# Kernel tuning notes

Hardware: AMD Instinct MI355X
Metric: run time of the kernel (lower is better)

## Reference

```python
import jax, jax.numpy as jnp
import numpy as np
import heapq

N = 256          # num nodes (also num start-node runs)
T = 5 * N        # message budget per run (graph.num_nodes * 5)
IN = 128         # in_features
H = 256          # hidden
M = 128          # message_size
OUT = 64         # out_features
E = 768          # directed edge list length (undirected adjacency built from it)


def _build_schedule(edge_index, n, t_max, rng):
    """Deterministically replay the heap simulation from the torch module.
    Returns proc[n,T] (node popped at each step), parent[n,T] (index of the
    step whose output message is consumed; -1 => first_message), valid[n,T]."""
    adj = [set() for _ in range(n)]
    src, dst = edge_index
    for s, d in zip(src, dst):
        adj[int(s)].add(int(d))
        adj[int(d)].add(int(s))
    adj = [sorted(a) for a in adj]
    proc = np.zeros((n, t_max), np.int32)
    parent = np.full((n, t_max), -1, np.int32)
    valid = np.zeros((n, t_max), bool)
    for i in range(n):
        heap = [(0.0, 0, i, -1)]  # (delay, tiebreak, node, parent_step)
        cnt = 1
        t = 0
        while heap and t < t_max:
            delay, _, node, par = heapq.heappop(heap)
            proc[i, t] = node
            parent[i, t] = par
            valid[i, t] = True
            for nb in adj[node]:
                nd = max(1e-10, rng.normal(0.5, 0.5))
                heapq.heappush(heap, (delay + nd, cnt, nb, t))
                cnt += 1
            t += 1
    return proc, parent, valid


def setup_inputs() -> dict:
    key = jax.random.key(0)
    ks = jax.random.split(key, 12)
    rng = np.random.default_rng(0)
    edge_index = rng.integers(0, N, size=(2, E))
    proc, parent, valid = _build_schedule(edge_index, N, T, rng)
    s = 0.05
    return {
        "x": jax.random.normal(ks[0], (N, IN), jnp.float32),
        "first_message": jnp.zeros((1, M), jnp.float32),
        "We": jax.random.normal(ks[1], (H, IN), jnp.float32) * s,
        "be": jax.random.normal(ks[2], (H,), jnp.float32) * s,
        "Ws": jax.random.normal(ks[3], (H, H + M), jnp.float32) * s,
        "bs": jax.random.normal(ks[4], (H,), jnp.float32) * s,
        "Wm": jax.random.normal(ks[5], (M, H + M), jnp.float32) * s,
        "bm": jax.random.normal(ks[6], (M,), jnp.float32) * s,
        "Wd": jax.random.normal(ks[7], (OUT, H), jnp.float32) * s,
        "bd": jax.random.normal(ks[8], (OUT,), jnp.float32) * s,
        "proc": jnp.asarray(proc),
        "parent": jnp.asarray(parent),
        "valid": jnp.asarray(valid),
    }


def reference(x, first_message, We, be, Ws, bs, Wm, bm, Wd, bd, proc, parent, valid):
    n = x.shape[0]
    t_max = proc.shape[1]
    m = first_message.shape[1]
    pred0 = x @ We.T + be  # encoder, recomputed fresh for every run -> shared [N,H]
    fmsg = first_message[0]

    def run(proc_i, parent_i, valid_i):
        msgs0 = jnp.zeros((t_max, m), x.dtype)

        def step(carry, inp):
            pred, msgs = carry
            t, node, par, v = inp
            msg = jnp.where(par < 0, fmsg, msgs[jnp.maximum(par, 0)])
            ns = jax.nn.relu(Ws @ jnp.concatenate([pred[node], msg]) + bs)
            nm = Wm @ jnp.concatenate([ns, msg]) + bm
            pred = pred.at[node].set(jnp.where(v, ns, pred[node]))
            msgs = msgs.at[t].set(jnp.where(v, nm, msgs[t]))
            return (pred, msgs), None

        (pred, _), _ = jax.lax.scan(
            step, (pred0, msgs0), (jnp.arange(t_max), proc_i, parent_i, valid_i)
        )
        return pred

    preds = jax.vmap(run)(proc, parent, valid)  # [N, N, H]
    diag = preds[jnp.arange(n), jnp.arange(n)]  # node i's state after run started at i
    return jax.nn.log_softmax(diag @ Wd.T + bd, axis=-1)  # [N, OUT]
```

## Files before the change

### kernel.cpp

```cpp
#include <hip/hip_runtime.h>
#include <stdint.h>

typedef _Float16 half_t;
typedef _Float16 half2_t __attribute__((ext_vector_type(2)));
typedef _Float16 half8_t __attribute__((ext_vector_type(8)));

#define NN   256
#define TT   1280
#define INF  128
#define HH   256
#define MM   128
#define OUTF 64
#define HM   384

#define THREADS 512

#define LDS_PRED    0
#define LDS_PROC    131072
#define LDS_PARENT  136192
#define LDS_FMSG    141312
#define LDS_V2      141568
#define LDS_DIAG32  143104
#define SMEM_BYTES  144128

#define WS_PRED0    0
#define WS_WSH      131072
#define WS_WMH      327680
#define WS_MSGS     425984

__device__ __forceinline__ float dot2f(half2_t a, half2_t b, float c) {
#if __has_builtin(__builtin_amdgcn_fdot2)
  return __builtin_amdgcn_fdot2(a, b, c, false);
#else
  return c + (float)a[0] * (float)b[0] + (float)a[1] * (float)b[1];
#endif
}

__global__ __launch_bounds__(256)
void prep_kernel(const float* __restrict__ Ws, const float* __restrict__ Wm,
                 half_t* __restrict__ WsH, half_t* __restrict__ WmH)
{
  const int i = blockIdx.x * 256 + threadIdx.x;
  if (i < HH * HM) WsH[i] = (half_t)Ws[i];
  else             WmH[i - HH * HM] = (half_t)Wm[i - HH * HM];
}

__global__ __launch_bounds__(256)
void enc_kernel(const float* __restrict__ x, const float* __restrict__ We,
                const float* __restrict__ be, half_t* __restrict__ pred0)
{
  __shared__ float xs[INF];
  const int n = blockIdx.x;
  const int hh = threadIdx.x;
  if (hh < INF) xs[hh] = x[n * INF + hh];
  __syncthreads();
  const float* w = We + hh * INF;
  float acc = be[hh];
#pragma unroll 16
  for (int k = 0; k < INF; ++k) acc += w[k] * xs[k];
  pred0[n * HH + hh] = (half_t)acc;
}

#define P1_CHUNK(BASE, WOFF)                                                   \
  _Pragma("unroll")                                                            \
  for (int j = 0; j < 8; ++j) {                                                \
    half8_t v = *(const half8_t*)((BASE) + j * 16);                            \
    a0 = dot2f(__builtin_shufflevector(v, v, 0, 1), w1[(WOFF) + j*4 + 0], a0); \
    a1 = dot2f(__builtin_shufflevector(v, v, 2, 3), w1[(WOFF) + j*4 + 1], a1); \
    a2 = dot2f(__builtin_shufflevector(v, v, 4, 5), w1[(WOFF) + j*4 + 2], a2); \
    a3 = dot2f(__builtin_shufflevector(v, v, 6, 7), w1[(WOFF) + j*4 + 3], a3); \
  }

__global__ __launch_bounds__(THREADS, 2)
void sim_kernel(const half_t* __restrict__ WsH, const float* __restrict__ bs,
                const half_t* __restrict__ WmH, const float* __restrict__ bm,
                const float* __restrict__ Wd, const float* __restrict__ bd,
                const float* __restrict__ fmsg,
                const int* __restrict__ proc, const int* __restrict__ parent,
                const half_t* __restrict__ pred0,
                half_t* __restrict__ msgs,
                float* __restrict__ out)
{
  extern __shared__ char smem[];
  half_t* lds_pred        = (half_t*)(smem + LDS_PRED);
  int* lds_proc           = (int*)(smem + LDS_PROC);
  int* lds_par            = (int*)(smem + LDS_PARENT);
  half_t* lds_fmsg        = (half_t*)(smem + LDS_FMSG);
  char* v2base            = smem + LDS_V2;
  float* lds_diag         = (float*)(smem + LDS_DIAG32);

  const int tid = threadIdx.x;
  const int run = blockIdx.x;
  const int r1 = tid >> 1, h = tid & 1;
  const int r2 = tid >> 2, q = tid & 3;

  half2_t w1[96];
  {
    const half8_t* wr = (const half8_t*)(WsH + r1 * HM + h * 192);
#pragma unroll
    for (int j = 0; j < 24; ++j) {
      half8_t v = wr[j];
      w1[4*j+0] = __builtin_shufflevector(v, v, 0, 1);
      w1[4*j+1] = __builtin_shufflevector(v, v, 2, 3);
      w1[4*j+2] = __builtin_shufflevector(v, v, 4, 5);
      w1[4*j+3] = __builtin_shufflevector(v, v, 6, 7);
    }
  }
  half2_t w2[48];
  {
    const half8_t* wr = (const half8_t*)(WmH + r2 * HM + q * 96);
#pragma unroll
    for (int j = 0; j < 12; ++j) {
      half8_t v = wr[j];
      w2[4*j+0] = __builtin_shufflevector(v, v, 0, 1);
      w2[4*j+1] = __builtin_shufflevector(v, v, 2, 3);
      w2[4*j+2] = __builtin_shufflevector(v, v, 4, 5);
      w2[4*j+3] = __builtin_shufflevector(v, v, 6, 7);
    }
  }
  const float bsv = bs[r1];
  const float bmv = bm[r2];

  {
    const uint4* s = (const uint4*)pred0;
    uint4* d = (uint4*)lds_pred;
#pragma unroll
    for (int i = 0; i < (NN * HH * 2 / 16) / THREADS; ++i)
      d[tid + i * THREADS] = s[tid + i * THREADS];
  }
  {
    const int* procR = proc + run * TT;
    const int* parR  = parent + run * TT;
    for (int i = tid; i < TT; i += THREADS) {
      lds_proc[i] = procR[i];
      lds_par[i]  = parR[i];
    }
  }
  if (tid < MM) lds_fmsg[tid] = (half_t)fmsg[tid];
  __syncthreads();

  float diag_reg = (h == 0) ? (float)lds_pred[run * HH + r1] : 0.f;
  half_t* msgs_run = msgs + (size_t)run * TT * MM;

  {
    const int p0 = lds_par[0];
    if (tid < 16) {
      uint4 v;
      if (p0 < 0) v = *(const uint4*)((const char*)lds_fmsg + tid * 16);
      else        v = *(const uint4*)((const char*)(msgs_run + (size_t)p0 * MM) + tid * 16);
      *(uint4*)(v2base + 512 + tid * 16) = v;
    }
  }
  __syncthreads();

  uint4 pfB = make_uint4(0, 0, 0, 0);

  int b = 0;
  for (int t = 0; t < TT; ++t, b ^= 1) {
    const int node  = lds_proc[t];
    const int vld   = (t == 0) | (lds_par[t] >= 0);
    const int parn1 = (t + 1 < TT) ? lds_par[t + 1] : -1;
    const int parn2 = (t + 2 < TT) ? lds_par[t + 2] : -1;

    const bool useA = (parn1 >= 0) && (parn1 == t - 1);
    uint4 pfA;
    if (tid < 16 && useA)
      pfA = *(const uint4*)((const char*)(msgs_run + (size_t)parn1 * MM) + tid * 16);

    const char* predrow = (const char*)(lds_pred + node * HH);
    const char* msgb    = v2base + b * 768 + 512;
    const char* b0 = h ? predrow + 384 : predrow;
    const char* b1 = h ? msgb          : predrow + 128;
    const char* b2 = h ? msgb + 128    : predrow + 256;

    float a0 = 0.f, a1 = 0.f, a2 = 0.f, a3 = 0.f;
    P1_CHUNK(b0, 0)
    P1_CHUNK(b1, 32)
    P1_CHUNK(b2, 64)
    float acc = (a0 + a1) + (a2 + a3);
    acc += __shfl_xor(acc, 1);
    const float ns_v = fmaxf(acc + bsv, 0.f);
    if (h == 0) {
      *((half_t*)(v2base + b * 768) + r1) = (half_t)ns_v;
      if (vld && node == run) diag_reg = ns_v;
    }

    if (t + 1 < TT && tid < 16) {
      char* dst = v2base + (b ^ 1) * 768 + 512 + tid * 16;
      if (parn1 < 0)
        *(uint4*)dst = *(const uint4*)((const char*)lds_fmsg + tid * 16);
      else if (parn1 != t)
        *(uint4*)dst = useA ? pfA : pfB;
    }

    if (tid < 16 && parn2 >= 0 && parn2 < t)
      pfB = *(const uint4*)((const char*)(msgs_run + (size_t)parn2 * MM) + tid * 16);

    __syncthreads();

    const char* vb = v2base + b * 768 + q * 192;
    float c0 = 0.f, c1 = 0.f, c2 = 0.f, c3 = 0.f;
#pragma unroll
    for (int j = 0; j < 12; ++j) {
      half8_t v = *(const half8_t*)(vb + j * 16);
      c0 = dot2f(__builtin_shufflevector(v, v, 0, 1), w2[j*4 + 0], c0);
      c1 = dot2f(__builtin_shufflevector(v, v, 2, 3), w2[j*4 + 1], c1);
      c2 = dot2f(__builtin_shufflevector(v, v, 4, 5), w2[j*4 + 2], c2);
      c3 = dot2f(__builtin_shufflevector(v, v, 6, 7), w2[j*4 + 3], c3);
    }
    float acc2 = (c0 + c1) + (c2 + c3);
    acc2 += __shfl_xor(acc2, 1);
    acc2 += __shfl_xor(acc2, 2);

    if (q == 0) {
      const float nm = acc2 + bmv;
      const half_t nmh = vld ? (half_t)nm : (half_t)0.f;
      if (vld) msgs_run[(size_t)t * MM + r2] = nmh;
      if (parn1 == t)
        *((half_t*)(v2base + (b ^ 1) * 768 + 512) + r2) = nmh;
    }
    if (h == 0 && vld)
      lds_pred[node * HH + r1] = (half_t)ns_v;
    __syncthreads();
  }

  if (h == 0) lds_diag[r1] = diag_reg;
  __syncthreads();

  if (tid < OUTF) {
    const float* wd = Wd + tid * HH;
    float acc = bd[tid];
#pragma unroll 8
    for (int k = 0; k < HH; ++k) acc += wd[k] * lds_diag[k];
    float m = acc;
#pragma unroll
    for (int off = 32; off >= 1; off >>= 1) m = fmaxf(m, __shfl_xor(m, off));
    const float e = __expf(acc - m);
    float s = e;
#pragma unroll
    for (int off = 32; off >= 1; off >>= 1) s += __shfl_xor(s, off);
    out[run * OUTF + tid] = acc - m - logf(s);
  }
}

extern "C" void kernel_launch(void* const* d_in, const int* in_sizes, int n_in,
                              void* d_out, int out_size, void* d_ws, size_t ws_size,
                              hipStream_t stream) {
  (void)in_sizes; (void)n_in; (void)out_size; (void)ws_size;
  const float* x    = (const float*)d_in[0];
  const float* fm   = (const float*)d_in[1];
  const float* We   = (const float*)d_in[2];
  const float* be   = (const float*)d_in[3];
  const float* Ws   = (const float*)d_in[4];
  const float* bs   = (const float*)d_in[5];
  const float* Wm   = (const float*)d_in[6];
  const float* bm   = (const float*)d_in[7];
  const float* Wd   = (const float*)d_in[8];
  const float* bd   = (const float*)d_in[9];
  const int* proc   = (const int*)d_in[10];
  const int* parent = (const int*)d_in[11];
  float* out = (float*)d_out;

  half_t* pred0 = (half_t*)((char*)d_ws + WS_PRED0);
  half_t* WsH   = (half_t*)((char*)d_ws + WS_WSH);
  half_t* WmH   = (half_t*)((char*)d_ws + WS_WMH);
  half_t* msgs  = (half_t*)((char*)d_ws + WS_MSGS);

  (void)hipFuncSetAttribute((const void*)sim_kernel,
                            hipFuncAttributeMaxDynamicSharedMemorySize, SMEM_BYTES);

  prep_kernel<<<dim3((HH * HM + MM * HM) / 256), dim3(256), 0, stream>>>(Ws, Wm, WsH, WmH);
  enc_kernel<<<dim3(NN), dim3(256), 0, stream>>>(x, We, be, pred0);
  sim_kernel<<<dim3(NN), dim3(THREADS), SMEM_BYTES, stream>>>(
      WsH, bs, WmH, bm, Wd, bd, fm, proc, parent, pred0, msgs, out);
}
```

Before: 1.885 ms.

## Remap GEMV threads to split K across 16 lanes with DPP row reductions

```diff
diff --git a/kernel.cpp b/kernel.cpp
--- a/kernel.cpp
+++ b/kernel.cpp
@@ -3,7 +3,6 @@
 
 typedef _Float16 half_t;
 typedef _Float16 half2_t __attribute__((ext_vector_type(2)));
-typedef _Float16 half8_t __attribute__((ext_vector_type(8)));
 
 #define NN   256
 #define TT   1280
@@ -20,8 +19,7 @@
 #define LDS_PARENT  136192
 #define LDS_FMSG    141312
 #define LDS_V2      141568
-#define LDS_DIAG32  143104
-#define SMEM_BYTES  144128
+#define SMEM_BYTES  143104
 
 #define WS_PRED0    0
 #define WS_WSH      131072
@@ -34,6 +32,20 @@
 #else
   return c + (float)a[0] * (float)b[0] + (float)a[1] * (float)b[1];
 #endif
+}
+
+template <int CTRL>
+__device__ __forceinline__ float dpp_add(float x) {
+  int xi = __float_as_int(x);
+  int yi = __builtin_amdgcn_update_dpp(xi, xi, CTRL, 0xf, 0xf, false);
+  return x + __int_as_float(yi);
+}
+__device__ __forceinline__ float row16_reduce(float x) {
+  x = dpp_add<0xB1>(x);
+  x = dpp_add<0x4E>(x);
+  x = dpp_add<0x141>(x);
+  x = dpp_add<0x140>(x);
+  return x;
 }
 
 __global__ __launch_bounds__(256)
@@ -60,16 +72,6 @@
   for (int k = 0; k < INF; ++k) acc += w[k] * xs[k];
   pred0[n * HH + hh] = (half_t)acc;
 }
-
-#define P1_CHUNK(BASE, WOFF)                                                   \
-  _Pragma("unroll")                                                            \
-  for (int j = 0; j < 8; ++j) {                                                \
-    half8_t v = *(const half8_t*)((BASE) + j * 16);                            \
-    a0 = dot2f(__builtin_shufflevector(v, v, 0, 1), w1[(WOFF) + j*4 + 0], a0); \
-    a1 = dot2f(__builtin_shufflevector(v, v, 2, 3), w1[(WOFF) + j*4 + 1], a1); \
-    a2 = dot2f(__builtin_shufflevector(v, v, 4, 5), w1[(WOFF) + j*4 + 2], a2); \
-    a3 = dot2f(__builtin_shufflevector(v, v, 6, 7), w1[(WOFF) + j*4 + 3], a3); \
-  }
 
 __global__ __launch_bounds__(THREADS, 2)
 void sim_kernel(const half_t* __restrict__ WsH, const float* __restrict__ bs,
@@ -87,39 +89,50 @@
   int* lds_par            = (int*)(smem + LDS_PARENT);
   half_t* lds_fmsg        = (half_t*)(smem + LDS_FMSG);
   char* v2base            = smem + LDS_V2;
-  float* lds_diag         = (float*)(smem + LDS_DIAG32);
-
-  const int tid = threadIdx.x;
-  const int run = blockIdx.x;
-  const int r1 = tid >> 1, h = tid & 1;
-  const int r2 = tid >> 2, q = tid & 3;
-
-  half2_t w1[96];
-  {
-    const half8_t* wr = (const half8_t*)(WsH + r1 * HM + h * 192);
-#pragma unroll
-    for (int j = 0; j < 24; ++j) {
-      half8_t v = wr[j];
-      w1[4*j+0] = __builtin_shufflevector(v, v, 0, 1);
-      w1[4*j+1] = __builtin_shufflevector(v, v, 2, 3);
-      w1[4*j+2] = __builtin_shufflevector(v, v, 4, 5);
-      w1[4*j+3] = __builtin_shufflevector(v, v, 6, 7);
-    }
-  }
-  half2_t w2[48];
-  {
-    const half8_t* wr = (const half8_t*)(WmH + r2 * HM + q * 96);
-#pragma unroll
-    for (int j = 0; j < 12; ++j) {
-      half8_t v = wr[j];
-      w2[4*j+0] = __builtin_shufflevector(v, v, 0, 1);
-      w2[4*j+1] = __builtin_shufflevector(v, v, 2, 3);
-      w2[4*j+2] = __builtin_shufflevector(v, v, 4, 5);
-      w2[4*j+3] = __builtin_shufflevector(v, v, 6, 7);
-    }
-  }
-  const float bsv = bs[r1];
-  const float bmv = bm[r2];
+
+  const int tid  = threadIdx.x;
+  const int run  = blockIdx.x;
+  const int wave = tid >> 6;
+  const int lane = tid & 63;
+  const int c    = lane & 15;
+  const int rg   = wave * 4 + (lane >> 4);
+  const int obyte = c * 48;
+
+  int w1i[96];
+  {
+    const char* wb = (const char*)WsH + (size_t)(rg * 8) * (HM * 2) + obyte;
+#pragma unroll
+    for (int r = 0; r < 8; ++r)
+#pragma unroll
+      for (int jj = 0; jj < 3; ++jj) {
+        int4 v = *(const int4*)(wb + r * (HM * 2) + jj * 16);
+        w1i[r * 12 + jj * 4 + 0] = v.x;
+        w1i[r * 12 + jj * 4 + 1] = v.y;
+        w1i[r * 12 + jj * 4 + 2] = v.z;
+        w1i[r * 12 + jj * 4 + 3] = v.w;
+      }
+  }
+  int w2i[48];
+  {
+    const char* wb = (const char*)WmH + (size_t)(rg * 4) * (HM * 2) + obyte;
+#pragma unroll
+    for (int r = 0; r < 4; ++r)
+#pragma unroll
+      for (int jj = 0; jj < 3; ++jj) {
+        int4 v = *(const int4*)(wb + r * (HM * 2) + jj * 16);
+        w2i[r * 12 + jj * 4 + 0] = v.x;
+        w2i[r * 12 + jj * 4 + 1] = v.y;
+        w2i[r * 12 + jj * 4 + 2] = v.z;
+        w2i[r * 12 + jj * 4 + 3] = v.w;
+      }
+  }
+#pragma unroll
+  for (int j = 0; j < 96; ++j) asm volatile("" : "+v"(w1i[j]));
+#pragma unroll
+  for (int j = 0; j < 48; ++j) asm volatile("" : "+v"(w2i[j]));
+
+  const float bs1 = (c < 8) ? bs[rg * 8 + c] : 0.f;
+  const float bm1 = (c < 4) ? bm[rg * 4 + c] : 0.f;
 
   {
     const uint4* s = (const uint4*)pred0;
@@ -139,7 +152,6 @@
   if (tid < MM) lds_fmsg[tid] = (half_t)fmsg[tid];
   __syncthreads();
 
-  float diag_reg = (h == 0) ? (float)lds_pred[run * HH + r1] : 0.f;
   half_t* msgs_run = msgs + (size_t)run * TT * MM;
 
   {
@@ -169,21 +181,46 @@
 
     const char* predrow = (const char*)(lds_pred + node * HH);
     const char* msgb    = v2base + b * 768 + 512;
-    const char* b0 = h ? predrow + 384 : predrow;
-    const char* b1 = h ? msgb          : predrow + 128;
-    const char* b2 = h ? msgb + 128    : predrow + 256;
-
-    float a0 = 0.f, a1 = 0.f, a2 = 0.f, a3 = 0.f;
-    P1_CHUNK(b0, 0)
-    P1_CHUNK(b1, 32)
-    P1_CHUNK(b2, 64)
-    float acc = (a0 + a1) + (a2 + a3);
-    acc += __shfl_xor(acc, 1);
-    const float ns_v = fmaxf(acc + bsv, 0.f);
-    if (h == 0) {
-      *((half_t*)(v2base + b * 768) + r1) = (half_t)ns_v;
-      if (vld && node == run) diag_reg = ns_v;
-    }
+    int av[12];
+    {
+#pragma unroll
+      for (int j = 0; j < 3; ++j) {
+        const int o = obyte + j * 16;
+        const char* p = (o < 512) ? (predrow + o) : (msgb + (o - 512));
+        int4 A = *(const int4*)p;
+        av[j * 4 + 0] = A.x; av[j * 4 + 1] = A.y;
+        av[j * 4 + 2] = A.z; av[j * 4 + 3] = A.w;
+      }
+    }
+    float acc0 = 0.f, acc1 = 0.f, acc2_ = 0.f, acc3 = 0.f;
+    float acc4 = 0.f, acc5 = 0.f, acc6 = 0.f, acc7 = 0.f;
+#pragma unroll
+    for (int k = 0; k < 12; ++k) {
+      const half2_t a = __builtin_bit_cast(half2_t, av[k]);
+      acc0 = dot2f(a, __builtin_bit_cast(half2_t, w1i[0 * 12 + k]), acc0);
+      acc1 = dot2f(a, __builtin_bit_cast(half2_t, w1i[1 * 12 + k]), acc1);
+      acc2_ = dot2f(a, __builtin_bit_cast(half2_t, w1i[2 * 12 + k]), acc2_);
+      acc3 = dot2f(a, __builtin_bit_cast(half2_t, w1i[3 * 12 + k]), acc3);
+      acc4 = dot2f(a, __builtin_bit_cast(half2_t, w1i[4 * 12 + k]), acc4);
+      acc5 = dot2f(a, __builtin_bit_cast(half2_t, w1i[5 * 12 + k]), acc5);
+      acc6 = dot2f(a, __builtin_bit_cast(half2_t, w1i[6 * 12 + k]), acc6);
+      acc7 = dot2f(a, __builtin_bit_cast(half2_t, w1i[7 * 12 + k]), acc7);
+    }
+    float nsv = 0.f;
+    {
+      float s;
+      s = row16_reduce(acc0); if (c == 0) nsv = s;
+      s = row16_reduce(acc1); if (c == 1) nsv = s;
+      s = row16_reduce(acc2_); if (c == 2) nsv = s;
+      s = row16_reduce(acc3); if (c == 3) nsv = s;
+      s = row16_reduce(acc4); if (c == 4) nsv = s;
+      s = row16_reduce(acc5); if (c == 5) nsv = s;
+      s = row16_reduce(acc6); if (c == 6) nsv = s;
+      s = row16_reduce(acc7); if (c == 7) nsv = s;
+    }
+    nsv = fmaxf(nsv + bs1, 0.f);
+    const half_t nsh = (half_t)nsv;
+    if (c < 8) ((half_t*)(v2base + b * 768))[rg * 8 + c] = nsh;
 
     if (t + 1 < TT && tid < 16) {
       char* dst = v2base + (b ^ 1) * 768 + 512 + tid * 16;
@@ -192,46 +229,56 @@
       else if (parn1 != t)
         *(uint4*)dst = useA ? pfA : pfB;
     }
-
     if (tid < 16 && parn2 >= 0 && parn2 < t)
       pfB = *(const uint4*)((const char*)(msgs_run + (size_t)parn2 * MM) + tid * 16);
 
     __syncthreads();
 
-    const char* vb = v2base + b * 768 + q * 192;
-    float c0 = 0.f, c1 = 0.f, c2 = 0.f, c3 = 0.f;
-#pragma unroll
-    for (int j = 0; j < 12; ++j) {
-      half8_t v = *(const half8_t*)(vb + j * 16);
-      c0 = dot2f(__builtin_shufflevector(v, v, 0, 1), w2[j*4 + 0], c0);
-      c1 = dot2f(__builtin_shufflevector(v, v, 2, 3), w2[j*4 + 1], c1);
-      c2 = dot2f(__builtin_shufflevector(v, v, 4, 5), w2[j*4 + 2], c2);
-      c3 = dot2f(__builtin_shufflevector(v, v, 6, 7), w2[j*4 + 3], c3);
-    }
-    float acc2 = (c0 + c1) + (c2 + c3);
-    acc2 += __shfl_xor(acc2, 1);
-    acc2 += __shfl_xor(acc2, 2);
-
-    if (q == 0) {
-      const float nm = acc2 + bmv;
-      const half_t nmh = vld ? (half_t)nm : (half_t)0.f;
-      if (vld) msgs_run[(size_t)t * MM + r2] = nmh;
+    const char* v2b = v2base + b * 768;
+    int bv[12];
+    {
+#pragma unroll
+      for (int j = 0; j < 3; ++j) {
+        int4 B = *(const int4*)(v2b + obyte + j * 16);
+        bv[j * 4 + 0] = B.x; bv[j * 4 + 1] = B.y;
+        bv[j * 4 + 2] = B.z; bv[j * 4 + 3] = B.w;
+      }
+    }
+    float m0 = 0.f, m1 = 0.f, m2 = 0.f, m3 = 0.f;
+#pragma unroll
+    for (int k = 0; k < 12; ++k) {
+      const half2_t a = __builtin_bit_cast(half2_t, bv[k]);
+      m0 = dot2f(a, __builtin_bit_cast(half2_t, w2i[0 * 12 + k]), m0);
+      m1 = dot2f(a, __builtin_bit_cast(half2_t, w2i[1 * 12 + k]), m1);
+      m2 = dot2f(a, __builtin_bit_cast(half2_t, w2i[2 * 12 + k]), m2);
+      m3 = dot2f(a, __builtin_bit_cast(half2_t, w2i[3 * 12 + k]), m3);
+    }
+    float nmv = 0.f;
+    {
+      float s;
+      s = row16_reduce(m0); if (c == 0) nmv = s;
+      s = row16_reduce(m1); if (c == 1) nmv = s;
+      s = row16_reduce(m2); if (c == 2) nmv = s;
+      s = row16_reduce(m3); if (c == 3) nmv = s;
+    }
+    if (c < 4) {
+      nmv += bm1;
+      const half_t nmh = vld ? (half_t)nmv : (half_t)0.f;
+      const int row2 = rg * 4 + c;
+      if (vld) msgs_run[(size_t)t * MM + row2] = nmh;
       if (parn1 == t)
-        *((half_t*)(v2base + (b ^ 1) * 768 + 512) + r2) = nmh;
-    }
-    if (h == 0 && vld)
-      lds_pred[node * HH + r1] = (half_t)ns_v;
+        ((half_t*)(v2base + (b ^ 1) * 768 + 512))[row2] = nmh;
+    }
+    if (c < 8 && vld)
+      lds_pred[node * HH + rg * 8 + c] = nsh;
     __syncthreads();
   }
-
-  if (h == 0) lds_diag[r1] = diag_reg;
-  __syncthreads();
 
   if (tid < OUTF) {
     const float* wd = Wd + tid * HH;
     float acc = bd[tid];
 #pragma unroll 8
-    for (int k = 0; k < HH; ++k) acc += wd[k] * lds_diag[k];
+    for (int k = 0; k < HH; ++k) acc += wd[k] * (float)lds_pred[run * HH + k];
     float m = acc;
 #pragma unroll
     for (int off = 32; off >= 1; off >>= 1) m = fmaxf(m, __shfl_xor(m, off));
```

New measurement: 2.003 ms. +6.2%, slower.
